# Optimization experiments

Hardware: AMD Instinct MI355X
Metric: run time of the kernel (lower is better)

Reference implementation:

```python
import jax, jax.numpy as jnp
import numpy as np

EPS = 1e-5

def setup_inputs() -> dict:
    key = jax.random.key(0)
    ks = jax.random.split(key, 8)
    N, D = 65536, 256
    x = jax.random.normal(ks[0], (N, D), dtype=jnp.float32)
    # BatchNorm1d affine params (frozen, torch default init)
    bn_gamma = jnp.ones((D,), jnp.float32)
    bn_beta = jnp.zeros((D,), jnp.float32)
    # Linear layers, torch default uniform(-1/sqrt(fan_in), 1/sqrt(fan_in))
    def lin(k, fin, fout):
        k1, k2 = jax.random.split(k)
        bound = 1.0 / np.sqrt(fin)
        W = jax.random.uniform(k1, (fout, fin), jnp.float32, -bound, bound)
        b = jax.random.uniform(k2, (fout,), jnp.float32, -bound, bound)
        return W, b
    W1, b1 = lin(ks[1], D, 512)
    W2, b2 = lin(ks[2], 512, 2048)
    Wf, bf = lin(ks[3], 2048, D)
    return {"x": x, "bn_gamma": bn_gamma, "bn_beta": bn_beta,
            "W1": W1, "b1": b1, "W2": W2, "b2": b2, "Wf": Wf, "bf": bf}


def reference(x, bn_gamma, bn_beta, W1, b1, W2, b2, Wf, bf):
    # BatchNorm1d in training mode: per-batch mean / biased variance
    mu = jnp.mean(x, axis=0)
    var = jnp.mean(jnp.square(x - mu), axis=0)
    xn = (x - mu) * jax.lax.rsqrt(var + EPS) * bn_gamma + bn_beta
    raw_feats = jnp.tanh(xn)
    h = xn @ W1.T + b1          # [N, 512]
    h = h @ W2.T + b2           # [N, 2048]
    out = jnp.tanh(h @ Wf.T + bf)  # [N, latent_dim]
    return (out, raw_feats)
```

## Files before the change

### kernel.cpp

```cpp
#include <hip/hip_runtime.h>
#include <hip/hip_bf16.h>
#include <stdint.h>

#define NROWS 65536
#define DFEAT 256

typedef __bf16 bf16x8 __attribute__((ext_vector_type(8)));
typedef float f32x4 __attribute__((ext_vector_type(4)));

__device__ __forceinline__ float fast_tanh(float x) {
    return 1.0f - 2.0f / (__expf(2.0f * x) + 1.0f);
}

__global__ void k1_kernel(const float4* __restrict__ x4,
                          float* __restrict__ sums,
                          float* __restrict__ sumsq,
                          const float* __restrict__ Wf,
                          const float* __restrict__ W2,
                          const float* __restrict__ b1,
                          const float* __restrict__ b2,
                          float* __restrict__ P,
                          float* __restrict__ u) {
    __shared__ float smem[2176];
    int t = threadIdx.x;
    int b = blockIdx.x;
    if (b < 512) {
        float (*ps)[256] = (float (*)[256])smem;
        float (*pq)[256] = (float (*)[256])(smem + 1024);
        int c4 = t & 63;
        int r  = t >> 6;
        size_t i0 = (size_t)b * 128;
        float4 s = make_float4(0.f, 0.f, 0.f, 0.f);
        float4 q = make_float4(0.f, 0.f, 0.f, 0.f);
        for (int i = r; i < 128; i += 4) {
            float4 v = x4[(i0 + i) * 64 + c4];
            s.x += v.x; s.y += v.y; s.z += v.z; s.w += v.w;
            q.x += v.x * v.x; q.y += v.y * v.y; q.z += v.z * v.z; q.w += v.w * v.w;
        }
        ps[r][c4 * 4 + 0] = s.x; ps[r][c4 * 4 + 1] = s.y;
        ps[r][c4 * 4 + 2] = s.z; ps[r][c4 * 4 + 3] = s.w;
        pq[r][c4 * 4 + 0] = q.x; pq[r][c4 * 4 + 1] = q.y;
        pq[r][c4 * 4 + 2] = q.z; pq[r][c4 * 4 + 3] = q.w;
        __syncthreads();
        float ts = ps[0][t] + ps[1][t] + ps[2][t] + ps[3][t];
        float tq = pq[0][t] + pq[1][t] + pq[2][t] + pq[3][t];
        atomicAdd(&sums[t], ts);
        atomicAdd(&sumsq[t], tq);
    } else if (b < 1024) {
        int bb = b - 512;
        int bj = (bb & 15) * 32;
        int bi = ((bb >> 4) & 7) * 32;
        int kb = (bb >> 7) * 512;
        float (*As)[33] = (float (*)[33])smem;
        float (*Bs)[33] = (float (*)[33])(smem + 1056);
        int tx = t & 15, ty = t >> 4;
        int row = t >> 3;
        int col = (t & 7) * 4;
        float acc00 = 0.f, acc01 = 0.f, acc10 = 0.f, acc11 = 0.f;
        for (int k0 = kb; k0 < kb + 512; k0 += 32) {
            float4 av = *(const float4*)&Wf[(size_t)(bi + row) * 2048 + k0 + col];
            As[row][col + 0] = av.x; As[row][col + 1] = av.y;
            As[row][col + 2] = av.z; As[row][col + 3] = av.w;
            float4 bv = *(const float4*)&W2[(size_t)(k0 + row) * 512 + bj + col];
            Bs[row][col + 0] = bv.x; Bs[row][col + 1] = bv.y;
            Bs[row][col + 2] = bv.z; Bs[row][col + 3] = bv.w;
            __syncthreads();
            #pragma unroll
            for (int k = 0; k < 32; ++k) {
                float a0 = As[ty * 2 + 0][k];
                float a1 = As[ty * 2 + 1][k];
                float b0 = Bs[k][tx * 2 + 0];
                float b1v = Bs[k][tx * 2 + 1];
                acc00 += a0 * b0; acc01 += a0 * b1v;
                acc10 += a1 * b0; acc11 += a1 * b1v;
            }
            __syncthreads();
        }
        int i = bi + ty * 2, j = bj + tx * 2;
        atomicAdd(&P[(size_t)(i + 0) * 512 + j + 0], acc00);
        atomicAdd(&P[(size_t)(i + 0) * 512 + j + 1], acc01);
        atomicAdd(&P[(size_t)(i + 1) * 512 + j + 0], acc10);
        atomicAdd(&P[(size_t)(i + 1) * 512 + j + 1], acc11);
    } else {
        int lane = t & 63;
        int row = (b - 1024) * 4 + (t >> 6);
        const float* Wr = W2 + (size_t)row * 512;
        float s = 0.f;
        for (int k = lane; k < 512; k += 64) s += Wr[k] * b1[k];
        #pragma unroll
        for (int off = 32; off; off >>= 1) s += __shfl_xor(s, off);
        if (lane == 0) u[row] = s + b2[row];
    }
}

__global__ void k2_kernel(const float* __restrict__ sums,
                          const float* __restrict__ sumsq,
                          const float* __restrict__ gamma,
                          const float* __restrict__ beta,
                          float* __restrict__ scl,
                          float* __restrict__ sft,
                          const float* __restrict__ P,
                          const float* __restrict__ W1,
                          const float* __restrict__ Wf,
                          const float* __restrict__ u,
                          const float* __restrict__ bfv,
                          __bf16* __restrict__ Bprep,
                          float* __restrict__ cv) {
    __shared__ float smem[2176];
    int t = threadIdx.x;
    int b = blockIdx.x;
    if (b >= 128) {
        const float invN = 1.0f / (float)NROWS;
        float mu  = sums[t] * invN;
        float var = sumsq[t] * invN - mu * mu;
        float rs  = rsqrtf(var + 1e-5f);
        float a   = gamma[t] * rs;
        scl[t] = a;
        sft[t] = beta[t] - mu * a;
        return;
    }
    if (b >= 64) {
        int lane = t & 63;
        int row = (b - 64) * 4 + (t >> 6);
        const float* Wr = Wf + (size_t)row * 2048;
        float s = 0.f;
        for (int k = lane; k < 2048; k += 64) s += Wr[k] * u[k];
        #pragma unroll
        for (int off = 32; off; off >>= 1) s += __shfl_xor(s, off);
        if (lane == 0) cv[row] = s + bfv[row];
        return;
    }
    float (*As)[33] = (float (*)[33])smem;
    float (*Bs)[33] = (float (*)[33])(smem + 1056);
    int tx = t & 15, ty = t >> 4;
    int bi = (b >> 3) * 32;
    int bj = (b & 7) * 32;
    int row = t >> 3;
    int col = (t & 7) * 4;
    float acc00 = 0.f, acc01 = 0.f, acc10 = 0.f, acc11 = 0.f;
    for (int k0 = 0; k0 < 512; k0 += 32) {
        float4 av = *(const float4*)&P[(size_t)(bi + row) * 512 + k0 + col];
        As[row][col + 0] = av.x; As[row][col + 1] = av.y;
        As[row][col + 2] = av.z; As[row][col + 3] = av.w;
        float4 bv = *(const float4*)&W1[(size_t)(k0 + row) * 256 + bj + col];
        Bs[row][col + 0] = bv.x; Bs[row][col + 1] = bv.y;
        Bs[row][col + 2] = bv.z; Bs[row][col + 3] = bv.w;
        __syncthreads();
        #pragma unroll
        for (int k = 0; k < 32; ++k) {
            float a0 = As[ty * 2 + 0][k];
            float a1 = As[ty * 2 + 1][k];
            float b0 = Bs[k][tx * 2 + 0];
            float b1v = Bs[k][tx * 2 + 1];
            acc00 += a0 * b0; acc01 += a0 * b1v;
            acc10 += a1 * b0; acc11 += a1 * b1v;
        }
        __syncthreads();
    }
    int j = bi + ty * 2, k = bj + tx * 2;
    float vals[2][2] = {{acc00, acc01}, {acc10, acc11}};
    #pragma unroll
    for (int dj = 0; dj < 2; ++dj)
        #pragma unroll
        for (int dk = 0; dk < 2; ++dk) {
            float v = vals[dj][dk];
            int jj = j + dj, kk = k + dk;
            __bf16 h = (__bf16)v;
            __bf16 lo = (__bf16)(v - (float)h);
            int kstep = kk >> 5, kgrp = (kk >> 3) & 3, e = kk & 7;
            Bprep[((((size_t)kstep * 2 + 0) * 4 + kgrp) * 256 + jj) * 8 + e] = h;
            Bprep[((((size_t)kstep * 2 + 1) * 4 + kgrp) * 256 + jj) * 8 + e] = lo;
        }
}

__global__ __launch_bounds__(256, 4)
void main_mfma(const float4* __restrict__ x4,
               const float4* __restrict__ scl4,
               const float4* __restrict__ sft4,
               const __bf16* __restrict__ Bprep,
               const float* __restrict__ cvec,
               float* __restrict__ out,
               float4* __restrict__ rf4) {
    __shared__ __align__(16) __bf16 Abuf[2][64][4][8];
    int t = threadIdx.x;
    int l = t & 63;
    int w = t >> 6;
    int g = l >> 4, li = l & 15;
    size_t row0 = (size_t)blockIdx.x * 64;
    int arow = t >> 2;
    int akg  = t & 3;

    f32x4 acc[4][4];
    #pragma unroll
    for (int i = 0; i < 4; ++i)
        #pragma unroll
        for (int j = 0; j < 4; ++j)
            acc[i][j] = (f32x4){0.f, 0.f, 0.f, 0.f};

    for (int s = 0; s < 8; ++s) {
        size_t xbase = (row0 + arow) * 64 + s * 8 + akg * 2;
        float4 v0 = x4[xbase];
        float4 v1 = x4[xbase + 1];
        int kb4 = s * 8 + akg * 2;
        float4 sc0 = scl4[kb4], sc1 = scl4[kb4 + 1];
        float4 sf0 = sft4[kb4], sf1 = sft4[kb4 + 1];
        float xn[8];
        xn[0] = v0.x * sc0.x + sf0.x;
        xn[1] = v0.y * sc0.y + sf0.y;
        xn[2] = v0.z * sc0.z + sf0.z;
        xn[3] = v0.w * sc0.w + sf0.w;
        xn[4] = v1.x * sc1.x + sf1.x;
        xn[5] = v1.y * sc1.y + sf1.y;
        xn[6] = v1.z * sc1.z + sf1.z;
        xn[7] = v1.w * sc1.w + sf1.w;
        float4 r0, r1;
        r0.x = fast_tanh(xn[0]); r0.y = fast_tanh(xn[1]);
        r0.z = fast_tanh(xn[2]); r0.w = fast_tanh(xn[3]);
        r1.x = fast_tanh(xn[4]); r1.y = fast_tanh(xn[5]);
        r1.z = fast_tanh(xn[6]); r1.w = fast_tanh(xn[7]);
        rf4[xbase] = r0;
        rf4[xbase + 1] = r1;
        bf16x8 hv, lv;
        #pragma unroll
        for (int e = 0; e < 8; ++e) {
            __bf16 h = (__bf16)xn[e];
            hv[e] = h;
            lv[e] = (__bf16)(xn[e] - (float)h);
        }
        *(bf16x8*)&Abuf[0][arow][akg][0] = hv;
        *(bf16x8*)&Abuf[1][arow][akg][0] = lv;
        __syncthreads();

        bf16x8 ah[4], al[4];
        #pragma unroll
        for (int i = 0; i < 4; ++i) {
            ah[i] = *(const bf16x8*)&Abuf[0][i * 16 + li][g][0];
            al[i] = *(const bf16x8*)&Abuf[1][i * 16 + li][g][0];
        }
        const __bf16* bh_base = Bprep + (size_t)(8 * s + g) * 2048;
        const __bf16* bl_base = Bprep + (size_t)(8 * s + 4 + g) * 2048;
        #pragma unroll
        for (int j = 0; j < 4; ++j) {
            int coll = w * 64 + j * 16 + li;
            bf16x8 bh = *(const bf16x8*)&bh_base[(size_t)coll * 8];
            bf16x8 bl = *(const bf16x8*)&bl_base[(size_t)coll * 8];
            #pragma unroll
            for (int i = 0; i < 4; ++i) {
                acc[i][j] = __builtin_amdgcn_mfma_f32_16x16x32_bf16(ah[i], bh, acc[i][j], 0, 0, 0);
                acc[i][j] = __builtin_amdgcn_mfma_f32_16x16x32_bf16(al[i], bh, acc[i][j], 0, 0, 0);
                acc[i][j] = __builtin_amdgcn_mfma_f32_16x16x32_bf16(ah[i], bl, acc[i][j], 0, 0, 0);
            }
        }
        __syncthreads();
    }

    #pragma unroll
    for (int j = 0; j < 4; ++j) {
        int gcol = w * 64 + j * 16 + li;
        float cj = cvec[gcol];
        #pragma unroll
        for (int i = 0; i < 4; ++i) {
            #pragma unroll
            for (int r = 0; r < 4; ++r) {
                size_t grow = row0 + i * 16 + g * 4 + r;
                out[grow * 256 + gcol] = fast_tanh(acc[i][j][r] + cj);
            }
        }
    }
}

extern "C" void kernel_launch(void* const* d_in, const int* in_sizes, int n_in,
                              void* d_out, int out_size, void* d_ws, size_t ws_size,
                              hipStream_t stream) {
    const float* x     = (const float*)d_in[0];
    const float* gamma = (const float*)d_in[1];
    const float* beta  = (const float*)d_in[2];
    const float* W1    = (const float*)d_in[3];
    const float* b1    = (const float*)d_in[4];
    const float* W2    = (const float*)d_in[5];
    const float* b2    = (const float*)d_in[6];
    const float* Wf    = (const float*)d_in[7];
    const float* bf    = (const float*)d_in[8];

    float* out = (float*)d_out;
    float* rf  = out + (size_t)NROWS * DFEAT;

    float* ws    = (float*)d_ws;
    float* sums  = ws;
    float* sumsq = ws + 256;
    float* P     = ws + 512;
    float* u     = ws + 131584;
    float* cv    = ws + 133632;
    float* scl   = ws + 133888;
    float* sft   = ws + 134144;
    __bf16* Bprep = (__bf16*)(ws + 134400);

    hipMemsetAsync(ws, 0, (size_t)131584 * sizeof(float), stream);

    k1_kernel<<<1536, 256, 0, stream>>>((const float4*)x, sums, sumsq,
                                        Wf, W2, b1, b2, P, u);
    k2_kernel<<<129, 256, 0, stream>>>(sums, sumsq, gamma, beta, scl, sft,
                                       P, W1, Wf, u, bf, Bprep, cv);
    main_mfma<<<NROWS / 64, 256, 0, stream>>>((const float4*)x,
                                              (const float4*)scl,
                                              (const float4*)sft,
                                              Bprep, cv, out, (float4*)rf);
}
```

Before: 258.5 us.

## Double-buffer A tile, prefetch next x slice, and cache BN scale/shift in LDS

The main MFMA kernel now double-buffers the LDS A tile, which removes the trailing barrier per k-step. It also issues the global load of the next x slice before the barrier so the load overlaps the MFMA work. The BN scale and shift vectors are staged once per block into shared memory instead of being reloaded from global memory every step. This adds LDS usage and live registers, which could affect occupancy under the 4-blocks launch bound.

Result: slower. 264.6 us (+2.4%).

```diff
diff --git a/kernel.cpp b/kernel.cpp
--- a/kernel.cpp
+++ b/kernel.cpp
@@ -175,13 +175,14 @@
 
 __global__ __launch_bounds__(256, 4)
 void main_mfma(const float4* __restrict__ x4,
-               const float4* __restrict__ scl4,
-               const float4* __restrict__ sft4,
+               const float* __restrict__ scl,
+               const float* __restrict__ sft,
                const __bf16* __restrict__ Bprep,
                const float* __restrict__ cvec,
                float* __restrict__ out,
                float4* __restrict__ rf4) {
-    __shared__ __align__(16) __bf16 Abuf[2][64][4][8];
+    __shared__ __align__(16) __bf16 Abuf[2][2][64][4][8];
+    __shared__ float ss[256], sh[256];
     int t = threadIdx.x;
     int l = t & 63;
     int w = t >> 6;
@@ -190,6 +191,9 @@
     int arow = t >> 2;
     int akg  = t & 3;
 
+    ss[t] = scl[t];
+    sh[t] = sft[t];
+
     f32x4 acc[4][4];
     #pragma unroll
     for (int i = 0; i < 4; ++i)
@@ -197,13 +201,17 @@
         for (int j = 0; j < 4; ++j)
             acc[i][j] = (f32x4){0.f, 0.f, 0.f, 0.f};
 
+    size_t xb = (row0 + arow) * 64 + akg * 2;
+    float4 v0 = x4[xb];
+    float4 v1 = x4[xb + 1];
+
+    __syncthreads();
+
+    #pragma unroll 2
     for (int s = 0; s < 8; ++s) {
-        size_t xbase = (row0 + arow) * 64 + s * 8 + akg * 2;
-        float4 v0 = x4[xbase];
-        float4 v1 = x4[xbase + 1];
-        int kb4 = s * 8 + akg * 2;
-        float4 sc0 = scl4[kb4], sc1 = scl4[kb4 + 1];
-        float4 sf0 = sft4[kb4], sf1 = sft4[kb4 + 1];
+        int kb = s * 32 + akg * 8;
+        float4 sc0 = *(const float4*)&ss[kb], sc1 = *(const float4*)&ss[kb + 4];
+        float4 sf0 = *(const float4*)&sh[kb], sf1 = *(const float4*)&sh[kb + 4];
         float xn[8];
         xn[0] = v0.x * sc0.x + sf0.x;
         xn[1] = v0.y * sc0.y + sf0.y;
@@ -218,8 +226,8 @@
         r0.z = fast_tanh(xn[2]); r0.w = fast_tanh(xn[3]);
         r1.x = fast_tanh(xn[4]); r1.y = fast_tanh(xn[5]);
         r1.z = fast_tanh(xn[6]); r1.w = fast_tanh(xn[7]);
-        rf4[xbase] = r0;
-        rf4[xbase + 1] = r1;
+        rf4[xb + s * 8] = r0;
+        rf4[xb + s * 8 + 1] = r1;
         bf16x8 hv, lv;
         #pragma unroll
         for (int e = 0; e < 8; ++e) {
@@ -227,15 +235,19 @@
             hv[e] = h;
             lv[e] = (__bf16)(xn[e] - (float)h);
         }
-        *(bf16x8*)&Abuf[0][arow][akg][0] = hv;
-        *(bf16x8*)&Abuf[1][arow][akg][0] = lv;
+        *(bf16x8*)&Abuf[s & 1][0][arow][akg][0] = hv;
+        *(bf16x8*)&Abuf[s & 1][1][arow][akg][0] = lv;
+        if (s < 7) {
+            v0 = x4[xb + (s + 1) * 8];
+            v1 = x4[xb + (s + 1) * 8 + 1];
+        }
         __syncthreads();
 
         bf16x8 ah[4], al[4];
         #pragma unroll
         for (int i = 0; i < 4; ++i) {
-            ah[i] = *(const bf16x8*)&Abuf[0][i * 16 + li][g][0];
-            al[i] = *(const bf16x8*)&Abuf[1][i * 16 + li][g][0];
+            ah[i] = *(const bf16x8*)&Abuf[s & 1][0][i * 16 + li][g][0];
+            al[i] = *(const bf16x8*)&Abuf[s & 1][1][i * 16 + li][g][0];
         }
         const __bf16* bh_base = Bprep + (size_t)(8 * s + g) * 2048;
         const __bf16* bl_base = Bprep + (size_t)(8 * s + 4 + g) * 2048;
@@ -251,7 +263,6 @@
                 acc[i][j] = __builtin_amdgcn_mfma_f32_16x16x32_bf16(ah[i], bl, acc[i][j], 0, 0, 0);
             }
         }
-        __syncthreads();
     }
 
     #pragma unroll
@@ -301,8 +312,6 @@
                                         Wf, W2, b1, b2, P, u);
     k2_kernel<<<129, 256, 0, stream>>>(sums, sumsq, gamma, beta, scl, sft,
                                        P, W1, Wf, u, bf, Bprep, cv);
-    main_mfma<<<NROWS / 64, 256, 0, stream>>>((const float4*)x,
-                                              (const float4*)scl,
-                                              (const float4*)sft,
+    main_mfma<<<NROWS / 64, 256, 0, stream>>>((const float4*)x, scl, sft,
                                               Bprep, cv, out, (float4*)rf);
 }
```
